# Kernel tuning notes

Hardware: AMD Instinct MI355X
Metric: run time of the kernel (lower is better)

## Reference

```python
import math
import jax, jax.numpy as jnp
import numpy as np

B, L, S, H, E = 4, 2048, 2048, 8, 64

def setup_inputs() -> dict:
    key = jax.random.key(0)
    kq, kk, kv, km = jax.random.split(key, 4)
    queries = jax.random.normal(kq, (B, L, H, E), dtype=jnp.float32)
    keys = jax.random.normal(kk, (B, S, H, E), dtype=jnp.float32)
    values = jax.random.normal(kv, (B, S, H, E), dtype=jnp.float32)
    # bool mask [B, L, S]; True => masked out (filled with -10000)
    attn_mask = jax.random.randint(km, (B, L, S), 0, 2).astype(bool)
    return {"queries": queries, "keys": keys, "values": values, "attn_mask": attn_mask}

def reference(queries, keys, values, attn_mask):
    # queries: [B,L,H,E], keys/values: [B,S,H,E], attn_mask: [B,L,S] bool
    Edim = queries.shape[-1]
    scale = 1.0 / math.sqrt(Edim)  # self.scale is None -> 1/sqrt(E)
    scores = jnp.einsum('blhe,bshe->bhls', queries, keys) * scale  # [B,H,L,S]
    scores = jnp.where(attn_mask[:, None, :, :], jnp.float32(-10000.0), scores)
    A = jax.nn.softmax(scores, axis=-1)  # dropout is identity at eval time
    V = jnp.einsum('bhls,bshd->blhd', A, values)  # [B,L,H,E]
    return V, A
```

## Files before the change

kernel.cpp:

```cpp
#include <hip/hip_runtime.h>


typedef __attribute__((ext_vector_type(8))) short bf16x8;
typedef __attribute__((ext_vector_type(4))) short bf16x4;
typedef __attribute__((ext_vector_type(4))) float f32x4;

#define NB 4
#define NL 2048
#define NS 2048
#define NH 8
#define NE 64
#define SKC 64
#define NT (NS / SKC)
#define SC2 0.18033688011112042f
#define MB2 -5.770780163555854f
#define EXP2(x) __builtin_amdgcn_exp2f(x)

static __device__ __forceinline__ short f2bf(float x) {
  unsigned u = __builtin_bit_cast(unsigned, x);
  u += 0x7fffu + ((u >> 16) & 1u);
  return (short)(u >> 16);
}

static __device__ __forceinline__ bf16x8 pack8(f32x4 a, f32x4 b) {
  bf16x8 t;
  t[0] = f2bf(a[0]); t[1] = f2bf(a[1]); t[2] = f2bf(a[2]); t[3] = f2bf(a[3]);
  t[4] = f2bf(b[0]); t[5] = f2bf(b[1]); t[6] = f2bf(b[2]); t[7] = f2bf(b[3]);
  return t;
}

__global__ __launch_bounds__(256)
void prep_all(const float* __restrict__ K, const float* __restrict__ V,
              const int* __restrict__ M, short* __restrict__ Kb,
              short* __restrict__ Vt, unsigned long long* __restrict__ Mb) {
  __shared__ short t_lds[64 * 65];
  const int bid = blockIdx.x, tid = threadIdx.x;
  if (bid < 4096) {
    long i4 = ((long)bid * 256 + tid) * 4;
    f32x4 v = *(const f32x4*)(K + i4);
    int e4 = (int)(i4 & 63);
    long r = i4 >> 6;
    int h = (int)(r & 7);
    long r2 = r >> 3;
    int t = (int)(r2 & 2047);
    int b = (int)(r2 >> 11);
    bf16x4 o;
    o[0] = f2bf(v[0]); o[1] = f2bf(v[1]); o[2] = f2bf(v[2]); o[3] = f2bf(v[3]);
    *(bf16x4*)(Kb + ((((long)b * NH + h) * NL + t) * NE + e4)) = o;
  } else if (bid < 5120) {
    const int vb = bid - 4096;
    const int b = vb >> 8;
    const int h = (vb >> 5) & 7;
    const int sb = (vb & 31) * 64;
    {
      const int s = tid >> 2, e0 = (tid & 3) * 16;
      const float* vp = V + ((((long)b * NS + sb + s) * NH + h) * NE + e0);
      #pragma unroll
      for (int j = 0; j < 4; ++j) {
        f32x4 u = *(const f32x4*)(vp + j * 4);
        #pragma unroll
        for (int r = 0; r < 4; ++r) t_lds[(e0 + j * 4 + r) * 65 + s] = f2bf(u[r]);
      }
    }
    __syncthreads();
    {
      const int e = tid >> 2, s0 = (tid & 3) * 16;
      short* op = Vt + (((long)b * NH + h) * NE + e) * NS + sb + s0;
      short tmp[16];
      #pragma unroll
      for (int j = 0; j < 16; ++j) tmp[j] = t_lds[e * 65 + s0 + j];
      *(bf16x8*)(op)     = *(bf16x8*)(tmp);
      *(bf16x8*)(op + 8) = *(bf16x8*)(tmp + 8);
    }
  } else {
    const long total = (long)NB * NL * NS;
    long g = (long)(bid - 5120) * 256 + tid;
    const long stride = 2048L * 256;
    for (; g < total; g += stride) {
      unsigned long long bal = __ballot(M[g] != 0);
      if ((tid & 63) == 0) Mb[g >> 6] = bal;
    }
  }
}


template<int RS>
static __device__ __forceinline__ void stage_tile(const short* __restrict__ base,
                                                  short* lds, int tid, int w) {
  #pragma unroll
  for (int c = 0; c < 2; ++c) {
    const int rr = (tid >> 3) + c * 32;
    const int gg = (tid & 7) ^ (rr & 7);
    const short* sp = base + (long)rr * RS + gg * 8;
    __builtin_amdgcn_global_load_lds(
        (const __attribute__((address_space(1))) void*)sp,
        (__attribute__((address_space(3))) void*)(void*)((char*)lds + c * 4096 + w * 1024),
        16, 0, 0);
  }
}

__global__ __launch_bounds__(256, 4)
void attn_main(const float* __restrict__ Qg, const short* __restrict__ Kb,
               const short* __restrict__ Vt, const unsigned long long* __restrict__ Mb,
               float* __restrict__ OutV, float* __restrict__ OutA)
{
  __shared__ short k_lds[2][SKC * 64];
  __shared__ short vt_lds[2][NE * 64];
  __shared__ short p_lds[4][16 * 64];

  const int bid = blockIdx.x;
  const int hh = bid & 7, qt = (bid >> 3) & 31, bb = bid >> 8;
  const int tid = threadIdx.x, w = tid >> 6, lane = tid & 63;
  const int lq = lane & 15, lg = lane >> 4;
  const int qw = qt * 64 + w * 16, qrow = qw + lq;

  const short* Kpan = Kb + (long)(bb * NH + hh) * NS * NE;
  const short* Vpan = Vt + (long)(bb * NH + hh) * NE * NS;

  bf16x8 qf0, qf1;
  {
    const float* qp = Qg + (((long)bb * NL + qrow) * NH + hh) * NE + 8 * lg;
    qf0 = pack8(*(const f32x4*)(qp),      *(const f32x4*)(qp + 4));
    qf1 = pack8(*(const f32x4*)(qp + 32), *(const f32x4*)(qp + 36));
  }

  const unsigned long long* mrow = Mb + ((long)bb * NL + qrow) * (NS / 64);

  float l0 = 0.f, l1 = 0.f, l2 = 0.f, l3 = 0.f;
  {
    short *k0 = &k_lds[0][0], *k1 = &k_lds[1][0];
    stage_tile<NE>(Kpan, k0, tid, w);
    unsigned long long mcur = mrow[0];
    asm volatile("s_waitcnt vmcnt(0)" ::: "memory");
    __builtin_amdgcn_s_barrier();
    for (int t = 0; t < NT; ++t) {
      if (t + 1 < NT) stage_tile<NE>(Kpan + (long)(t + 1) * SKC * NE, k1, tid, w);
      const unsigned long long mnext = mrow[t + 1 < NT ? t + 1 : NT - 1];
      #pragma unroll
      for (int st = 0; st < SKC; st += 16) {
        const int krow = st + lq, sw = (krow & 7) << 3;
        const bf16x8 kf0 = *(const bf16x8*)&k0[(krow * 64 + 8 * lg) ^ sw];
        const bf16x8 kf1 = *(const bf16x8*)&k0[(krow * 64 + 32 + 8 * lg) ^ sw];
        f32x4 c = {0.f, 0.f, 0.f, 0.f};
        c = __builtin_amdgcn_mfma_f32_16x16x32_bf16(kf0, qf0, c, 0, 0, 0);
        c = __builtin_amdgcn_mfma_f32_16x16x32_bf16(kf1, qf1, c, 0, 0, 0);
        const unsigned mb4 = (unsigned)(mcur >> (st + 4 * lg)) & 0xFu;
        l0 += (mb4 & 1u) ? 0.f : EXP2(fmaf(c[0], SC2, MB2));
        l1 += (mb4 & 2u) ? 0.f : EXP2(fmaf(c[1], SC2, MB2));
        l2 += (mb4 & 4u) ? 0.f : EXP2(fmaf(c[2], SC2, MB2));
        l3 += (mb4 & 8u) ? 0.f : EXP2(fmaf(c[3], SC2, MB2));
      }
      mcur = mnext;
      if (t + 1 < NT)
        asm volatile("s_waitcnt vmcnt(1)" ::: "memory");
      __builtin_amdgcn_s_barrier();
      short* tk = k0; k0 = k1; k1 = tk;
    }
  }
  float l = (l0 + l1) + (l2 + l3);
  l += __shfl_xor(l, 16, 64);
  l += __shfl_xor(l, 32, 64);
  const float rinv = 1.0f / l;

  f32x4 accv[4];
  #pragma unroll
  for (int et = 0; et < 4; ++et) accv[et] = (f32x4){0.f, 0.f, 0.f, 0.f};

  float* arow = OutA + (((long)(bb * NH + hh)) * NL + qrow) * NS;
  {
    short *k0 = &k_lds[0][0], *k1 = &k_lds[1][0];
    short *v0 = &vt_lds[0][0], *v1 = &vt_lds[1][0];
    stage_tile<NE>(Kpan, k0, tid, w);
    stage_tile<NS>(Vpan, v0, tid, w);
    unsigned long long mcur = mrow[0];
    asm volatile("s_waitcnt vmcnt(0)" ::: "memory");
    __builtin_amdgcn_s_barrier();
    for (int t = 0; t < NT; ++t) {
      if (t + 1 < NT) {
        stage_tile<NE>(Kpan + (long)(t + 1) * SKC * NE, k1, tid, w);
        stage_tile<NS>(Vpan + (t + 1) * SKC, v1, tid, w);
      }
      const unsigned long long mnext = mrow[t + 1 < NT ? t + 1 : NT - 1];
      const int sb = t * SKC;
      #pragma unroll
      for (int st = 0; st < SKC; st += 16) {
        const int krow = st + lq, sw = (krow & 7) << 3;
        const bf16x8 kf0 = *(const bf16x8*)&k0[(krow * 64 + 8 * lg) ^ sw];
        const bf16x8 kf1 = *(const bf16x8*)&k0[(krow * 64 + 32 + 8 * lg) ^ sw];
        f32x4 c = {0.f, 0.f, 0.f, 0.f};
        c = __builtin_amdgcn_mfma_f32_16x16x32_bf16(kf0, qf0, c, 0, 0, 0);
        c = __builtin_amdgcn_mfma_f32_16x16x32_bf16(kf1, qf1, c, 0, 0, 0);
        const unsigned mb4 = (unsigned)(mcur >> (st + 4 * lg)) & 0xFu;
        const float p0 = (mb4 & 1u) ? 0.f : EXP2(fmaf(c[0], SC2, MB2));
        const float p1 = (mb4 & 2u) ? 0.f : EXP2(fmaf(c[1], SC2, MB2));
        const float p2 = (mb4 & 4u) ? 0.f : EXP2(fmaf(c[2], SC2, MB2));
        const float p3 = (mb4 & 8u) ? 0.f : EXP2(fmaf(c[3], SC2, MB2));
        const float a0 = p0 * rinv, a1 = p1 * rinv, a2 = p2 * rinv, a3 = p3 * rinv;
        f32x4 av = {a0, a1, a2, a3};
        __builtin_nontemporal_store(av, (f32x4*)(arow + sb + st + 4 * lg));
        bf16x4 pv;
        pv[0] = f2bf(a0); pv[1] = f2bf(a1); pv[2] = f2bf(a2); pv[3] = f2bf(a3);
        *(bf16x4*)&p_lds[w][(lq * 64 + st + 4 * lg) ^ ((lq & 7) << 3)] = pv;
      }
      #pragma unroll
      for (int kc2 = 0; kc2 < 2; ++kc2) {
        const bf16x8 pf = *(const bf16x8*)&p_lds[w][(lq * 64 + kc2 * 32 + 8 * lg) ^ ((lq & 7) << 3)];
        #pragma unroll
        for (int et = 0; et < 4; ++et) {
          const int er = et * 16 + lq;
          const bf16x8 vf = *(const bf16x8*)&v0[(er * 64 + kc2 * 32 + 8 * lg) ^ ((er & 7) << 3)];
          accv[et] = __builtin_amdgcn_mfma_f32_16x16x32_bf16(pf, vf, accv[et], 0, 0, 0);
        }
      }
      mcur = mnext;
      if (t + 1 < NT)
        asm volatile("s_waitcnt vmcnt(5)" ::: "memory");
      __builtin_amdgcn_s_barrier();
      short* tk = k0; k0 = k1; k1 = tk;
      short* tv = v0; v0 = v1; v1 = tv;
    }
  }

  {
    float* vout = OutV + (((long)bb * NL + qw + 4 * lg) * NH + hh) * NE + lq;
    #pragma unroll
    for (int r = 0; r < 4; ++r)
      #pragma unroll
      for (int et = 0; et < 4; ++et)
        vout[(long)r * (NH * NE) + et * 16] = accv[et][r];
  }
}

extern "C" void kernel_launch(void* const* d_in, const int* in_sizes, int n_in,
                              void* d_out, int out_size, void* d_ws, size_t ws_size,
                              hipStream_t stream) {
  const float* Q = (const float*)d_in[0];
  const float* K = (const float*)d_in[1];
  const float* V = (const float*)d_in[2];
  const int*   M = (const int*)d_in[3];
  float* outv = (float*)d_out;
  float* outa = outv + (size_t)NB * NL * NH * NE;

  const size_t NQK = (size_t)NB * NH * NL * NE;
  short* Kbw = (short*)d_ws;
  short* Vtw = Kbw + NQK;
  unsigned long long* Mbp = (unsigned long long*)(Vtw + NQK);

  prep_all<<<dim3(7168), 256, 0, stream>>>(K, V, M, Kbw, Vtw, Mbp);
  attn_main<<<dim3(NB * (NL / 64) * NH), 256, 0, stream>>>(Q, Kbw, Vtw, Mbp, outv, outa);
}
```

Measured before the change: 190.9 us.

## Load V fragments directly into registers and fold normalization into exp2 bias

Drops the LDS double-buffer for the transposed V panel. Each wave now loads its own V MFMA fragments from global memory into registers at the start of every S-tile, so only K is staged through LDS. Softmax normalization moves into the exponent by subtracting log2(l) from the bias, which removes the per-element multiply by 1/l. The cost is that each wave loads the same V data again, relying on cache hits, and that global-load latency is exposed at the start of each iteration.

```diff
diff --git a/kernel.cpp b/kernel.cpp
--- a/kernel.cpp
+++ b/kernel.cpp
@@ -84,14 +84,13 @@
 }
 
 
-template<int RS>
-static __device__ __forceinline__ void stage_tile(const short* __restrict__ base,
-                                                  short* lds, int tid, int w) {
+static __device__ __forceinline__ void stage_k(const short* __restrict__ base,
+                                               short* lds, int tid, int w) {
   #pragma unroll
   for (int c = 0; c < 2; ++c) {
     const int rr = (tid >> 3) + c * 32;
     const int gg = (tid & 7) ^ (rr & 7);
-    const short* sp = base + (long)rr * RS + gg * 8;
+    const short* sp = base + (long)rr * NE + gg * 8;
     __builtin_amdgcn_global_load_lds(
         (const __attribute__((address_space(1))) void*)sp,
         (__attribute__((address_space(3))) void*)(void*)((char*)lds + c * 4096 + w * 1024),
@@ -105,7 +104,6 @@
                float* __restrict__ OutV, float* __restrict__ OutA)
 {
   __shared__ short k_lds[2][SKC * 64];
-  __shared__ short vt_lds[2][NE * 64];
   __shared__ short p_lds[4][16 * 64];
 
   const int bid = blockIdx.x;
@@ -116,6 +114,7 @@
 
   const short* Kpan = Kb + (long)(bb * NH + hh) * NS * NE;
   const short* Vpan = Vt + (long)(bb * NH + hh) * NE * NS;
+  const short* vfrag = Vpan + (long)lq * NS + 8 * lg;
 
   bf16x8 qf0, qf1;
   {
@@ -129,12 +128,12 @@
   float l0 = 0.f, l1 = 0.f, l2 = 0.f, l3 = 0.f;
   {
     short *k0 = &k_lds[0][0], *k1 = &k_lds[1][0];
-    stage_tile<NE>(Kpan, k0, tid, w);
+    stage_k(Kpan, k0, tid, w);
     unsigned long long mcur = mrow[0];
     asm volatile("s_waitcnt vmcnt(0)" ::: "memory");
     __builtin_amdgcn_s_barrier();
     for (int t = 0; t < NT; ++t) {
-      if (t + 1 < NT) stage_tile<NE>(Kpan + (long)(t + 1) * SKC * NE, k1, tid, w);
+      if (t + 1 < NT) stage_k(Kpan + (long)(t + 1) * SKC * NE, k1, tid, w);
       const unsigned long long mnext = mrow[t + 1 < NT ? t + 1 : NT - 1];
       #pragma unroll
       for (int st = 0; st < SKC; st += 16) {
@@ -160,7 +159,7 @@
   float l = (l0 + l1) + (l2 + l3);
   l += __shfl_xor(l, 16, 64);
   l += __shfl_xor(l, 32, 64);
-  const float rinv = 1.0f / l;
+  const float mb2l = MB2 - __builtin_amdgcn_logf(l);
 
   f32x4 accv[4];
   #pragma unroll
@@ -169,19 +168,21 @@
   float* arow = OutA + (((long)(bb * NH + hh)) * NL + qrow) * NS;
   {
     short *k0 = &k_lds[0][0], *k1 = &k_lds[1][0];
-    short *v0 = &vt_lds[0][0], *v1 = &vt_lds[1][0];
-    stage_tile<NE>(Kpan, k0, tid, w);
-    stage_tile<NS>(Vpan, v0, tid, w);
+    stage_k(Kpan, k0, tid, w);
     unsigned long long mcur = mrow[0];
     asm volatile("s_waitcnt vmcnt(0)" ::: "memory");
     __builtin_amdgcn_s_barrier();
     for (int t = 0; t < NT; ++t) {
-      if (t + 1 < NT) {
-        stage_tile<NE>(Kpan + (long)(t + 1) * SKC * NE, k1, tid, w);
-        stage_tile<NS>(Vpan + (t + 1) * SKC, v1, tid, w);
-      }
+      const int sb = t * SKC;
+      bf16x8 vf[8];
+      #pragma unroll
+      for (int kc2 = 0; kc2 < 2; ++kc2)
+        #pragma unroll
+        for (int et = 0; et < 4; ++et)
+          vf[kc2 * 4 + et] =
+              *(const bf16x8*)(vfrag + (long)(et * 16) * NS + sb + kc2 * 32);
+      if (t + 1 < NT) stage_k(Kpan + (long)(t + 1) * SKC * NE, k1, tid, w);
       const unsigned long long mnext = mrow[t + 1 < NT ? t + 1 : NT - 1];
-      const int sb = t * SKC;
       #pragma unroll
       for (int st = 0; st < SKC; st += 16) {
         const int krow = st + lq, sw = (krow & 7) << 3;
@@ -191,11 +192,10 @@
         c = __builtin_amdgcn_mfma_f32_16x16x32_bf16(kf0, qf0, c, 0, 0, 0);
         c = __builtin_amdgcn_mfma_f32_16x16x32_bf16(kf1, qf1, c, 0, 0, 0);
         const unsigned mb4 = (unsigned)(mcur >> (st + 4 * lg)) & 0xFu;
-        const float p0 = (mb4 & 1u) ? 0.f : EXP2(fmaf(c[0], SC2, MB2));
-        const float p1 = (mb4 & 2u) ? 0.f : EXP2(fmaf(c[1], SC2, MB2));
-        const float p2 = (mb4 & 4u) ? 0.f : EXP2(fmaf(c[2], SC2, MB2));
-        const float p3 = (mb4 & 8u) ? 0.f : EXP2(fmaf(c[3], SC2, MB2));
-        const float a0 = p0 * rinv, a1 = p1 * rinv, a2 = p2 * rinv, a3 = p3 * rinv;
+        const float a0 = (mb4 & 1u) ? 0.f : EXP2(fmaf(c[0], SC2, mb2l));
+        const float a1 = (mb4 & 2u) ? 0.f : EXP2(fmaf(c[1], SC2, mb2l));
+        const float a2 = (mb4 & 4u) ? 0.f : EXP2(fmaf(c[2], SC2, mb2l));
+        const float a3 = (mb4 & 8u) ? 0.f : EXP2(fmaf(c[3], SC2, mb2l));
         f32x4 av = {a0, a1, a2, a3};
         __builtin_nontemporal_store(av, (f32x4*)(arow + sb + st + 4 * lg));
         bf16x4 pv;
@@ -206,18 +206,14 @@
       for (int kc2 = 0; kc2 < 2; ++kc2) {
         const bf16x8 pf = *(const bf16x8*)&p_lds[w][(lq * 64 + kc2 * 32 + 8 * lg) ^ ((lq & 7) << 3)];
         #pragma unroll
-        for (int et = 0; et < 4; ++et) {
-          const int er = et * 16 + lq;
-          const bf16x8 vf = *(const bf16x8*)&v0[(er * 64 + kc2 * 32 + 8 * lg) ^ ((er & 7) << 3)];
-          accv[et] = __builtin_amdgcn_mfma_f32_16x16x32_bf16(pf, vf, accv[et], 0, 0, 0);
-        }
+        for (int et = 0; et < 4; ++et)
+          accv[et] = __builtin_amdgcn_mfma_f32_16x16x32_bf16(pf, vf[kc2 * 4 + et], accv[et], 0, 0, 0);
       }
       mcur = mnext;
       if (t + 1 < NT)
         asm volatile("s_waitcnt vmcnt(5)" ::: "memory");
       __builtin_amdgcn_s_barrier();
       short* tk = k0; k0 = k1; k1 = tk;
-      short* tv = v0; v0 = v1; v1 = tv;
     }
   }
 
```

Result: slower. 224.8 us (+17.7%).

## Stage fp32 attention tile in LDS for coalesced row-contiguous A stores

Applied to the files above, without the earlier changes.

The probability tile is now written in fp32 to a padded per-wave LDS buffer and read back so each group of 16 lanes stores 256 contiguous bytes of one A row, instead of each lane writing 16-byte pieces scattered across rows. The PV MFMA operand is rebuilt from the same fp32 buffer by converting to bf16 after reading. This aims to cut the cost of the large A output write (B*H*L*S floats) by making stores coalesced. In exchange, LDS use roughly doubles for that buffer, occupancy in launch bounds is lowered from 4 to 3, and sched_barriers are added after the prefetch issue.

```diff
diff --git a/kernel.cpp b/kernel.cpp
--- a/kernel.cpp
+++ b/kernel.cpp
@@ -12,6 +12,7 @@
 #define NE 64
 #define SKC 64
 #define NT (NS / SKC)
+#define AW 68
 #define SC2 0.18033688011112042f
 #define MB2 -5.770780163555854f
 #define EXP2(x) __builtin_amdgcn_exp2f(x)
@@ -99,14 +100,14 @@
   }
 }
 
-__global__ __launch_bounds__(256, 4)
+__global__ __launch_bounds__(256, 3)
 void attn_main(const float* __restrict__ Qg, const short* __restrict__ Kb,
                const short* __restrict__ Vt, const unsigned long long* __restrict__ Mb,
                float* __restrict__ OutV, float* __restrict__ OutA)
 {
   __shared__ short k_lds[2][SKC * 64];
   __shared__ short vt_lds[2][NE * 64];
-  __shared__ short p_lds[4][16 * 64];
+  __shared__ float a_lds[4][16 * AW];
 
   const int bid = blockIdx.x;
   const int hh = bid & 7, qt = (bid >> 3) & 31, bb = bid >> 8;
@@ -135,6 +136,7 @@
     __builtin_amdgcn_s_barrier();
     for (int t = 0; t < NT; ++t) {
       if (t + 1 < NT) stage_tile<NE>(Kpan + (long)(t + 1) * SKC * NE, k1, tid, w);
+      __builtin_amdgcn_sched_barrier(0);
       const unsigned long long mnext = mrow[t + 1 < NT ? t + 1 : NT - 1];
       #pragma unroll
       for (int st = 0; st < SKC; st += 16) {
@@ -166,7 +168,7 @@
   #pragma unroll
   for (int et = 0; et < 4; ++et) accv[et] = (f32x4){0.f, 0.f, 0.f, 0.f};
 
-  float* arow = OutA + (((long)(bb * NH + hh)) * NL + qrow) * NS;
+  float* abase = OutA + ((long)(bb * NH + hh) * NL + qw) * NS;
   {
     short *k0 = &k_lds[0][0], *k1 = &k_lds[1][0];
     short *v0 = &vt_lds[0][0], *v1 = &vt_lds[1][0];
@@ -176,12 +178,13 @@
     asm volatile("s_waitcnt vmcnt(0)" ::: "memory");
     __builtin_amdgcn_s_barrier();
     for (int t = 0; t < NT; ++t) {
+      const int sb = t * SKC;
       if (t + 1 < NT) {
         stage_tile<NE>(Kpan + (long)(t + 1) * SKC * NE, k1, tid, w);
         stage_tile<NS>(Vpan + (t + 1) * SKC, v1, tid, w);
       }
+      __builtin_amdgcn_sched_barrier(0);
       const unsigned long long mnext = mrow[t + 1 < NT ? t + 1 : NT - 1];
-      const int sb = t * SKC;
       #pragma unroll
       for (int st = 0; st < SKC; st += 16) {
         const int krow = st + lq, sw = (krow & 7) << 3;
@@ -191,20 +194,27 @@
         c = __builtin_amdgcn_mfma_f32_16x16x32_bf16(kf0, qf0, c, 0, 0, 0);
         c = __builtin_amdgcn_mfma_f32_16x16x32_bf16(kf1, qf1, c, 0, 0, 0);
         const unsigned mb4 = (unsigned)(mcur >> (st + 4 * lg)) & 0xFu;
-        const float p0 = (mb4 & 1u) ? 0.f : EXP2(fmaf(c[0], SC2, MB2));
-        const float p1 = (mb4 & 2u) ? 0.f : EXP2(fmaf(c[1], SC2, MB2));
-        const float p2 = (mb4 & 4u) ? 0.f : EXP2(fmaf(c[2], SC2, MB2));
-        const float p3 = (mb4 & 8u) ? 0.f : EXP2(fmaf(c[3], SC2, MB2));
-        const float a0 = p0 * rinv, a1 = p1 * rinv, a2 = p2 * rinv, a3 = p3 * rinv;
-        f32x4 av = {a0, a1, a2, a3};
-        __builtin_nontemporal_store(av, (f32x4*)(arow + sb + st + 4 * lg));
-        bf16x4 pv;
-        pv[0] = f2bf(a0); pv[1] = f2bf(a1); pv[2] = f2bf(a2); pv[3] = f2bf(a3);
-        *(bf16x4*)&p_lds[w][(lq * 64 + st + 4 * lg) ^ ((lq & 7) << 3)] = pv;
+        f32x4 av;
+        av[0] = (mb4 & 1u) ? 0.f : EXP2(fmaf(c[0], SC2, MB2)) * rinv;
+        av[1] = (mb4 & 2u) ? 0.f : EXP2(fmaf(c[1], SC2, MB2)) * rinv;
+        av[2] = (mb4 & 4u) ? 0.f : EXP2(fmaf(c[2], SC2, MB2)) * rinv;
+        av[3] = (mb4 & 8u) ? 0.f : EXP2(fmaf(c[3], SC2, MB2)) * rinv;
+        *(f32x4*)&a_lds[w][lq * AW + st + 4 * lg] = av;
+      }
+      {
+        const int rr = lane >> 4, ls = lane & 15;
+        #pragma unroll
+        for (int it = 0; it < 4; ++it) {
+          const int r = it * 4 + rr;
+          const f32x4 a4 = *(const f32x4*)&a_lds[w][r * AW + ls * 4];
+          __builtin_nontemporal_store(a4, (f32x4*)(abase + (long)r * NS + sb + ls * 4));
+        }
       }
       #pragma unroll
       for (int kc2 = 0; kc2 < 2; ++kc2) {
-        const bf16x8 pf = *(const bf16x8*)&p_lds[w][(lq * 64 + kc2 * 32 + 8 * lg) ^ ((lq & 7) << 3)];
+        const f32x4 u0 = *(const f32x4*)&a_lds[w][lq * AW + kc2 * 32 + 8 * lg];
+        const f32x4 u1 = *(const f32x4*)&a_lds[w][lq * AW + kc2 * 32 + 8 * lg + 4];
+        const bf16x8 pf = pack8(u0, u1);
         #pragma unroll
         for (int et = 0; et < 4; ++et) {
           const int er = et * 16 + lq;
```

Result: no change. 190.9 us (-0.0%).
